# Kernel optimization log

Measured on AMD Instinct MI355X. Metric: run time of the kernel, lower is better.

Reference implementation:

```python
import jax, jax.numpy as jnp
import numpy as np

B, T, I, H, O = 32, 2048, 128, 512, 128
FORGET_BIAS = 1.0


def setup_inputs() -> dict:
    key = jax.random.key(0)
    ks = jax.random.split(key, 8)
    s_ih = 1.0 / np.sqrt(H)
    data = jax.random.normal(ks[0], (B, T, I), dtype=jnp.float32)
    h0 = jnp.zeros((B, H), dtype=jnp.float32)
    c0 = jnp.zeros((B, H), dtype=jnp.float32)
    W_ih = jax.random.uniform(ks[1], (4 * H, I), minval=-s_ih, maxval=s_ih, dtype=jnp.float32)
    W_hh = jax.random.uniform(ks[2], (4 * H, H), minval=-s_ih, maxval=s_ih, dtype=jnp.float32)
    b_ih = jax.random.uniform(ks[3], (4 * H,), minval=-s_ih, maxval=s_ih, dtype=jnp.float32)
    b_hh = jax.random.uniform(ks[4], (4 * H,), minval=-s_ih, maxval=s_ih, dtype=jnp.float32)
    # forget-gate bias init: slice [H:2H] of each bias filled with forget_bias/2
    b_ih = b_ih.at[H:2 * H].set(FORGET_BIAS / 2)
    b_hh = b_hh.at[H:2 * H].set(FORGET_BIAS / 2)
    lin_W = jax.random.uniform(ks[5], (O, H), minval=-s_ih, maxval=s_ih, dtype=jnp.float32)
    lin_b = jax.random.uniform(ks[6], (O,), minval=-s_ih, maxval=s_ih, dtype=jnp.float32)
    return dict(data=data, h0=h0, c0=c0, W_ih=W_ih, W_hh=W_hh,
                b_ih=b_ih, b_hh=b_hh, lin_W=lin_W, lin_b=lin_b)


def reference(data, h0, c0, W_ih, W_hh, b_ih, b_hh, lin_W, lin_b):
    # LSTMCell loop over time (batch_first). PyTorch gate order: i, f, g, o.
    # Original code appends the CELL state (variable `hidden` = c) to hs and
    # decodes from the stacked cell states — reproduced faithfully.
    bias = b_ih + b_hh  # [4H]

    def step(carry, x_t):
        h, c = carry
        gates = x_t @ W_ih.T + h @ W_hh.T + bias  # [B, 4H]
        i_g, f_g, g_g, o_g = jnp.split(gates, 4, axis=-1)
        c_new = jax.nn.sigmoid(f_g) * c + jax.nn.sigmoid(i_g) * jnp.tanh(g_g)
        h_new = jax.nn.sigmoid(o_g) * jnp.tanh(c_new)
        return (h_new, c_new), c_new

    xs = jnp.swapaxes(data, 0, 1)  # [T, B, I]
    (h_f, c_f), cs = jax.lax.scan(step, (h0, c0), xs)
    output = jnp.swapaxes(cs, 0, 1)  # [B, T, H]
    decoded = output @ lin_W.T + lin_b  # [B, T, O]
    return decoded, h_f, c_f
```

## Files before the change

kernel.cpp:

```cpp
#include <hip/hip_runtime.h>
#include <hip/hip_bf16.h>


#define B_ 32
#define T_ 2048
#define I_ 128
#define H_ 512
#define O_ 128
#define NG 8
#define BPG 4
#define WPG 32
#define NWG 256
#define NTHR 512
#define NBUF 4

#define HXS 656
#define CPS 520
#define CAN 0xAAAAAAAAu

typedef short bf16x8 __attribute__((ext_vector_type(8)));
typedef float f32x4 __attribute__((ext_vector_type(4)));
typedef unsigned long long u64;

static __device__ __forceinline__ unsigned f2bf(float f) {
  unsigned u = __float_as_uint(f);
  u = u + 0x7FFFu + ((u >> 16) & 1u);
  return u >> 16;
}
static __device__ __forceinline__ float bf2f(unsigned h) {
  return __uint_as_float(h << 16);
}
static __device__ __forceinline__ float fsigm(float x) {
  return 1.0f / (1.0f + __expf(-x));
}
static __device__ __forceinline__ float ftanh(float x) {
  return 1.0f - 2.0f / (__expf(2.0f * x) + 1.0f);
}

#define ALD(p) __hip_atomic_load((p), __ATOMIC_RELAXED, __HIP_MEMORY_SCOPE_AGENT)
#define AST(p, v) __hip_atomic_store((p), (v), __ATOMIC_RELAXED, __HIP_MEMORY_SCOPE_AGENT)
#define BARRIER() asm volatile("s_waitcnt lgkmcnt(0)\ns_barrier" ::: "memory")

__global__ __launch_bounds__(NTHR, 2) void lstm_fused(
    const float* __restrict__ data, const float* __restrict__ h0,
    const float* __restrict__ c0, const float* __restrict__ W_ih,
    const float* __restrict__ W_hh, const float* __restrict__ b_ih,
    const float* __restrict__ b_hh, const float* __restrict__ lin_W,
    const float* __restrict__ lin_b, float* __restrict__ out,
    float* __restrict__ ws) {
  __shared__ alignas(16) unsigned short sHxHi[BPG * HXS];
  __shared__ alignas(16) unsigned short sHxLo[BPG * HXS];
  __shared__ alignas(16) float sCp[2][BPG * CPS];
  __shared__ alignas(16) float sLinW[4 * CPS];
  __shared__ alignas(16) float sGates[4][2][68];
  __shared__ float sLinB[4];

  const int bid = blockIdx.x;
  const int g = bid & 7;
  const int wgi = bid >> 3;
  const int b0 = g * BPG;
  const int ubase = wgi * 16;
  const int tid = threadIdx.x;
  const int lane = tid & 63;
  const int w = tid >> 6;
  const int gate = w >> 1;
  const int kh = w & 1;
  const int m16 = lane & 15;
  const int kcg = lane >> 4;

  u64* hcPk = (u64*)ws;
  int* cnt = (int*)(ws + (size_t)NBUF * NG * BPG * H_ * 2);

  bf16x8 fAhi[10], fAlo[10];
  const int grow = gate * H_ + ubase + m16;
#pragma unroll
  for (int kk = 0; kk < 10; kk++) {
    int k = kh * 320 + kk * 32 + kcg * 8;
    const float* src = (k < H_) ? (W_hh + (size_t)grow * H_ + k)
                                : (W_ih + (size_t)grow * I_ + (k - H_));
    float4 v0 = *(const float4*)src;
    float4 v1 = *(const float4*)(src + 4);
    float w8[8] = {v0.x, v0.y, v0.z, v0.w, v1.x, v1.y, v1.z, v1.w};
    union { unsigned short u[8]; bf16x8 v; } hi, lo;
#pragma unroll
    for (int j = 0; j < 8; j++) {
      unsigned h = f2bf(w8[j]);
      hi.u[j] = (unsigned short)h;
      lo.u[j] = (unsigned short)f2bf(w8[j] - bf2f(h));
    }
    fAhi[kk] = hi.v;
    fAlo[kk] = lo.v;
  }
  float bias_[4], c_state = 0.f;
  if (tid < 64) {
    int up = tid >> 2, b = tid & 3;
#pragma unroll
    for (int ga = 0; ga < 4; ga++) {
      int r = ga * H_ + ubase + up;
      bias_[ga] = b_ih[r] + b_hh[r];
    }
    c_state = c0[(size_t)(b0 + b) * H_ + ubase + up];
  }
  for (int idx = tid; idx < 4 * H_; idx += NTHR) {
    int o = idx >> 9, k = idx & (H_ - 1);
    sLinW[o * CPS + k] = lin_W[(size_t)(wgi * 4 + o) * H_ + k];
  }
  if (tid < 4) sLinB[tid] = lin_b[wgi * 4 + tid];

  if (tid < 256) {
    int b = tid >> 6, off = (tid & 63) * 8;
    const float* src = h0 + (size_t)(b0 + b) * H_ + off;
    float4 v0 = *(const float4*)src;
    float4 v1 = *(const float4*)(src + 4);
    float w8[8] = {v0.x, v0.y, v0.z, v0.w, v1.x, v1.y, v1.z, v1.w};
    union { unsigned short u[8]; uint4 q; } hi, lo;
#pragma unroll
    for (int j = 0; j < 8; j++) {
      unsigned h = f2bf(w8[j]);
      hi.u[j] = (unsigned short)h;
      lo.u[j] = (unsigned short)f2bf(w8[j] - bf2f(h));
    }
    *(uint4*)&sHxHi[b * HXS + off] = hi.q;
    *(uint4*)&sHxLo[b * HXS + off] = lo.q;
  }
  if (tid >= 256 && tid < 384) {
    int i = tid - 256, b = i >> 5, c4 = i & 31;
    float4 v = *(const float4*)(data + ((size_t)(b0 + b) * T_) * I_ + c4 * 4);
    float w4[4] = {v.x, v.y, v.z, v.w};
    union { unsigned short u[4]; uint2 q; } hi, lo;
#pragma unroll
    for (int j = 0; j < 4; j++) {
      unsigned h = f2bf(w4[j]);
      hi.u[j] = (unsigned short)h;
      lo.u[j] = (unsigned short)f2bf(w4[j] - bf2f(h));
    }
    *(uint2*)&sHxHi[b * HXS + H_ + c4 * 4] = hi.q;
    *(uint2*)&sHxLo[b * HXS + H_ + c4 * 4] = lo.q;
  }
  float4 pfx;
  if (tid >= 320 && tid < 448) {
    int i = tid - 320, b = i >> 5, c4 = i & 31;
    int tp = (T_ > 1) ? 1 : 0;
    pfx = *(const float4*)(data + ((size_t)(b0 + b) * T_ + tp) * I_ + c4 * 4);
  }
  if (tid < 256) {
    int buf = tid >> 6, q = tid & 63, up = q >> 2, b = q & 3;
    AST(&hcPk[(((size_t)buf * NG + g) * BPG + b) * H_ + ubase + up],
        0xAAAAAAAAAAAAAAAAull);
  }
  asm volatile("s_waitcnt vmcnt(0)" ::: "memory");
  __syncthreads();
  if (tid == 0)
    __hip_atomic_fetch_add(&cnt[g * 16], 1, __ATOMIC_RELAXED,
                           __HIP_MEMORY_SCOPE_AGENT);
  if (tid < 64) {
    while (ALD(&cnt[g * 16]) < WPG) {}
  }
  __syncthreads();

  const int bcl = (m16 < BPG) ? m16 : (BPG - 1);
  const unsigned short* pBhi = sHxHi + bcl * HXS + kh * 320 + kcg * 8;
  const unsigned short* pBlo = sHxLo + bcl * HXS + kh * 320 + kcg * 8;

  for (int t = 0; t < T_; t++) {
    f32x4 a0 = {0.f, 0.f, 0.f, 0.f}, a1 = a0, a2 = a0;
#pragma unroll
    for (int kk = 0; kk < 10; kk++) {
      bf16x8 bh = *(const bf16x8*)(pBhi + kk * 32);
      bf16x8 bl = *(const bf16x8*)(pBlo + kk * 32);
      a0 = __builtin_amdgcn_mfma_f32_16x16x32_bf16(fAhi[kk], bh, a0, 0, 0, 0);
      a1 = __builtin_amdgcn_mfma_f32_16x16x32_bf16(fAhi[kk], bl, a1, 0, 0, 0);
      a2 = __builtin_amdgcn_mfma_f32_16x16x32_bf16(fAlo[kk], bh, a2, 0, 0, 0);
    }
    if (m16 < BPG) {
#pragma unroll
      for (int j = 0; j < 4; j++) {
        sGates[gate][kh][kcg * 16 + j * 4 + m16] = a0[j] + a1[j] + a2[j];
      }
    }
    BARRIER();

    if (tid < 64) {
      int up = tid >> 2, b = tid & 3;
      float gi = sGates[0][0][tid] + sGates[0][1][tid] + bias_[0];
      float gf = sGates[1][0][tid] + sGates[1][1][tid] + bias_[1];
      float gg = sGates[2][0][tid] + sGates[2][1][tid] + bias_[2];
      float go = sGates[3][0][tid] + sGates[3][1][tid] + bias_[3];
      float cn = fsigm(gf) * c_state + fsigm(gi) * ftanh(gg);
      float hn = fsigm(go) * ftanh(cn);
      c_state = cn;
      unsigned hh = f2bf(hn);
      unsigned hl = f2bf(hn - bf2f(hh));
      u64 pay = ((u64)__float_as_uint(cn) << 32) | (u64)((hh << 16) | hl);
      AST(&hcPk[(((size_t)(t & 3) * NG + g) * BPG + b) * H_ + ubase + up], pay);
      if (t == T_ - 1) {
        const size_t DEC = (size_t)B_ * T_ * O_;
        out[DEC + (size_t)(b0 + b) * H_ + ubase + up] = hn;
        out[DEC + (size_t)B_ * H_ + (size_t)(b0 + b) * H_ + ubase + up] = cn;
      }
    } else if (tid < 320) {
      if (t > 0) {
        int q = (tid >> 4) - 4;
        int ks = tid & 15;
        int o = q >> 2, b = q & 3;
        const float* cp = sCp[(t & 1) ^ 1];
        float s = 0.f;
#pragma unroll
        for (int j = 0; j < 32; j++) {
          int k = ks + j * 16;
          s += sLinW[o * CPS + k] * cp[b * CPS + k];
        }
        s += __shfl_xor(s, 1);
        s += __shfl_xor(s, 2);
        s += __shfl_xor(s, 4);
        s += __shfl_xor(s, 8);
        if (ks == 0)
          out[((size_t)(b0 + b) * T_ + (t - 1)) * O_ + wgi * 4 + o] =
              s + sLinB[o];
      }
    } else if (tid < 448) {
      int i = tid - 320, b = i >> 5, c4 = i & 31;
      union { unsigned short u[4]; uint2 q; } hi, lo;
      float w4[4] = {pfx.x, pfx.y, pfx.z, pfx.w};
#pragma unroll
      for (int j = 0; j < 4; j++) {
        unsigned h = f2bf(w4[j]);
        hi.u[j] = (unsigned short)h;
        lo.u[j] = (unsigned short)f2bf(w4[j] - bf2f(h));
      }
      *(uint2*)&sHxHi[b * HXS + H_ + c4 * 4] = hi.q;
      *(uint2*)&sHxLo[b * HXS + H_ + c4 * 4] = lo.q;
      int tp = (t + 2 < T_) ? t + 2 : T_ - 1;
      pfx = *(const float4*)(data + ((size_t)(b0 + b) * T_ + tp) * I_ + c4 * 4);
    } else {
      if (t >= 2) {
        int q = tid - 448, up7 = q >> 2, b7 = q & 3;
        AST(&hcPk[(((size_t)((t - 2) & 3) * NG + g) * BPG + b7) * H_ + ubase +
                  up7],
            0xAAAAAAAAAAAAAAAAull);
        asm volatile("s_waitcnt vmcnt(0)" ::: "memory");
      }
    }

    {
      int b = tid >> 7, u4 = (tid & 127) * 4;
      const u64* sp =
          hcPk + (((size_t)(t & 3) * NG + g) * BPG + b) * H_ + u4;
      u64 v0, v1, v2, v3;
      for (;;) {
        v0 = ALD(sp);
        v1 = ALD(sp + 1);
        v2 = ALD(sp + 2);
        v3 = ALD(sp + 3);
        if (((unsigned)v0 != CAN) & ((unsigned)v1 != CAN) &
            ((unsigned)v2 != CAN) & ((unsigned)v3 != CAN))
          break;
      }
      unsigned p0 = (unsigned)v0, p1 = (unsigned)v1, p2 = (unsigned)v2,
               p3 = (unsigned)v3;
      uint2 hw = {(p0 >> 16) | (p1 & 0xFFFF0000u),
                  (p2 >> 16) | (p3 & 0xFFFF0000u)};
      uint2 lw = {(p0 & 0xFFFFu) | (p1 << 16),
                  (p2 & 0xFFFFu) | (p3 << 16)};
      *(uint2*)&sHxHi[b * HXS + u4] = hw;
      *(uint2*)&sHxLo[b * HXS + u4] = lw;
      float4 cf = {__uint_as_float((unsigned)(v0 >> 32)),
                   __uint_as_float((unsigned)(v1 >> 32)),
                   __uint_as_float((unsigned)(v2 >> 32)),
                   __uint_as_float((unsigned)(v3 >> 32))};
      *(float4*)&sCp[t & 1][b * CPS + u4] = cf;
    }
    BARRIER();
  }

  {
    int q = tid >> 5, ks = tid & 31, o = q >> 2, b = q & 3;
    const float* cp = sCp[(T_ - 1) & 1];
    float s = 0.f;
#pragma unroll
    for (int j = 0; j < 16; j++) {
      int k = ks + j * 32;
      s += sLinW[o * CPS + k] * cp[b * CPS + k];
    }
    s += __shfl_xor(s, 1);
    s += __shfl_xor(s, 2);
    s += __shfl_xor(s, 4);
    s += __shfl_xor(s, 8);
    s += __shfl_xor(s, 16);
    if (ks == 0)
      out[((size_t)(b0 + b) * T_ + (T_ - 1)) * O_ + wgi * 4 + o] =
          s + sLinB[o];
  }
}

extern "C" void kernel_launch(void* const* d_in, const int* in_sizes, int n_in,
                              void* d_out, int out_size, void* d_ws, size_t ws_size,
                              hipStream_t stream) {
  const float* data = (const float*)d_in[0];
  const float* h0 = (const float*)d_in[1];
  const float* c0 = (const float*)d_in[2];
  const float* W_ih = (const float*)d_in[3];
  const float* W_hh = (const float*)d_in[4];
  const float* b_ih = (const float*)d_in[5];
  const float* b_hh = (const float*)d_in[6];
  const float* lin_W = (const float*)d_in[7];
  const float* lin_b = (const float*)d_in[8];
  float* out = (float*)d_out;
  float* ws = (float*)d_ws;

  const size_t CNT_OFF = (size_t)NBUF * NG * BPG * H_ * 8;
  hipMemsetAsync((char*)d_ws + CNT_OFF, 0, NG * 16 * sizeof(int), stream);

  hipLaunchKernelGGL(lstm_fused, dim3(NWG), dim3(NTHR), 0, stream, data, h0, c0,
                     W_ih, W_hh, b_ih, b_hh, lin_W, lin_b, out, ws);
}
```

Baseline: 5.505 ms.

## Replace canary-reset handoff with epoch tags embedded in cell-state bits

The cross-workgroup h/c exchange now marks each packed value with a 2-bit epoch tag stored in the low mantissa bits of the cell state, instead of polling for a canary pattern. This removes the per-step canary reset stores and their waitcnt, the startup counter barrier, and the host memset. The first poll loads are also issued right after the MFMA loop so their latency overlaps the gate epilogue. In exchange, the cell values used for decoding lose two mantissa bits. Correctness relies on stale workspace contents not carrying a matching tag.

New measurement: 5.917 ms. 1.07x slower.

```diff
diff --git a/kernel.cpp b/kernel.cpp
--- a/kernel.cpp
+++ b/kernel.cpp
@@ -16,7 +16,6 @@
 
 #define HXS 656
 #define CPS 520
-#define CAN 0xAAAAAAAAu
 
 typedef short bf16x8 __attribute__((ext_vector_type(8)));
 typedef float f32x4 __attribute__((ext_vector_type(4)));
@@ -69,7 +68,6 @@
   const int kcg = lane >> 4;
 
   u64* hcPk = (u64*)ws;
-  int* cnt = (int*)(ws + (size_t)NBUF * NG * BPG * H_ * 2);
 
   bf16x8 fAhi[10], fAlo[10];
   const int grow = gate * H_ + ubase + m16;
@@ -143,19 +141,6 @@
     int tp = (T_ > 1) ? 1 : 0;
     pfx = *(const float4*)(data + ((size_t)(b0 + b) * T_ + tp) * I_ + c4 * 4);
   }
-  if (tid < 256) {
-    int buf = tid >> 6, q = tid & 63, up = q >> 2, b = q & 3;
-    AST(&hcPk[(((size_t)buf * NG + g) * BPG + b) * H_ + ubase + up],
-        0xAAAAAAAAAAAAAAAAull);
-  }
-  asm volatile("s_waitcnt vmcnt(0)" ::: "memory");
-  __syncthreads();
-  if (tid == 0)
-    __hip_atomic_fetch_add(&cnt[g * 16], 1, __ATOMIC_RELAXED,
-                           __HIP_MEMORY_SCOPE_AGENT);
-  if (tid < 64) {
-    while (ALD(&cnt[g * 16]) < WPG) {}
-  }
   __syncthreads();
 
   const int bcl = (m16 < BPG) ? m16 : (BPG - 1);
@@ -163,6 +148,7 @@
   const unsigned short* pBlo = sHxLo + bcl * HXS + kh * 320 + kcg * 8;
 
   for (int t = 0; t < T_; t++) {
+    const unsigned tag = (unsigned)(((t >> 2) + 1) & 3);
     f32x4 a0 = {0.f, 0.f, 0.f, 0.f}, a1 = a0, a2 = a0;
 #pragma unroll
     for (int kk = 0; kk < 10; kk++) {
@@ -172,6 +158,12 @@
       a1 = __builtin_amdgcn_mfma_f32_16x16x32_bf16(fAhi[kk], bl, a1, 0, 0, 0);
       a2 = __builtin_amdgcn_mfma_f32_16x16x32_bf16(fAlo[kk], bh, a2, 0, 0, 0);
     }
+
+    const int sb = tid >> 7;
+    const int su4 = (tid & 127) * 4;
+    const u64* sp = hcPk + (((size_t)(t & 3) * NG + g) * BPG + sb) * H_ + su4;
+    u64 v0 = ALD(sp), v1 = ALD(sp + 1), v2 = ALD(sp + 2), v3 = ALD(sp + 3);
+
     if (m16 < BPG) {
 #pragma unroll
       for (int j = 0; j < 4; j++) {
@@ -191,7 +183,8 @@
       c_state = cn;
       unsigned hh = f2bf(hn);
       unsigned hl = f2bf(hn - bf2f(hh));
-      u64 pay = ((u64)__float_as_uint(cn) << 32) | (u64)((hh << 16) | hl);
+      unsigned cbits = (__float_as_uint(cn) & ~3u) | tag;
+      u64 pay = ((u64)cbits << 32) | (u64)((hh << 16) | hl);
       AST(&hcPk[(((size_t)(t & 3) * NG + g) * BPG + b) * H_ + ubase + up], pay);
       if (t == T_ - 1) {
         const size_t DEC = (size_t)B_ * T_ * O_;
@@ -232,43 +225,33 @@
       *(uint2*)&sHxLo[b * HXS + H_ + c4 * 4] = lo.q;
       int tp = (t + 2 < T_) ? t + 2 : T_ - 1;
       pfx = *(const float4*)(data + ((size_t)(b0 + b) * T_ + tp) * I_ + c4 * 4);
-    } else {
-      if (t >= 2) {
-        int q = tid - 448, up7 = q >> 2, b7 = q & 3;
-        AST(&hcPk[(((size_t)((t - 2) & 3) * NG + g) * BPG + b7) * H_ + ubase +
-                  up7],
-            0xAAAAAAAAAAAAAAAAull);
-        asm volatile("s_waitcnt vmcnt(0)" ::: "memory");
-      }
-    }
-
+    }
+
+    for (;;) {
+      bool bad = (((unsigned)(v0 >> 32) & 3) != tag) |
+                 (((unsigned)(v1 >> 32) & 3) != tag) |
+                 (((unsigned)(v2 >> 32) & 3) != tag) |
+                 (((unsigned)(v3 >> 32) & 3) != tag);
+      if (!bad) break;
+      v0 = ALD(sp);
+      v1 = ALD(sp + 1);
+      v2 = ALD(sp + 2);
+      v3 = ALD(sp + 3);
+    }
     {
-      int b = tid >> 7, u4 = (tid & 127) * 4;
-      const u64* sp =
-          hcPk + (((size_t)(t & 3) * NG + g) * BPG + b) * H_ + u4;
-      u64 v0, v1, v2, v3;
-      for (;;) {
-        v0 = ALD(sp);
-        v1 = ALD(sp + 1);
-        v2 = ALD(sp + 2);
-        v3 = ALD(sp + 3);
-        if (((unsigned)v0 != CAN) & ((unsigned)v1 != CAN) &
-            ((unsigned)v2 != CAN) & ((unsigned)v3 != CAN))
-          break;
-      }
       unsigned p0 = (unsigned)v0, p1 = (unsigned)v1, p2 = (unsigned)v2,
                p3 = (unsigned)v3;
       uint2 hw = {(p0 >> 16) | (p1 & 0xFFFF0000u),
                   (p2 >> 16) | (p3 & 0xFFFF0000u)};
       uint2 lw = {(p0 & 0xFFFFu) | (p1 << 16),
                   (p2 & 0xFFFFu) | (p3 << 16)};
-      *(uint2*)&sHxHi[b * HXS + u4] = hw;
-      *(uint2*)&sHxLo[b * HXS + u4] = lw;
-      float4 cf = {__uint_as_float((unsigned)(v0 >> 32)),
-                   __uint_as_float((unsigned)(v1 >> 32)),
-                   __uint_as_float((unsigned)(v2 >> 32)),
-                   __uint_as_float((unsigned)(v3 >> 32))};
-      *(float4*)&sCp[t & 1][b * CPS + u4] = cf;
+      *(uint2*)&sHxHi[sb * HXS + su4] = hw;
+      *(uint2*)&sHxLo[sb * HXS + su4] = lw;
+      float4 cf = {__uint_as_float((unsigned)(v0 >> 32) & ~3u),
+                   __uint_as_float((unsigned)(v1 >> 32) & ~3u),
+                   __uint_as_float((unsigned)(v2 >> 32) & ~3u),
+                   __uint_as_float((unsigned)(v3 >> 32) & ~3u)};
+      *(float4*)&sCp[t & 1][sb * CPS + su4] = cf;
     }
     BARRIER();
   }
@@ -308,9 +291,6 @@
   float* out = (float*)d_out;
   float* ws = (float*)d_ws;
 
-  const size_t CNT_OFF = (size_t)NBUF * NG * BPG * H_ * 8;
-  hipMemsetAsync((char*)d_ws + CNT_OFF, 0, NG * 16 * sizeof(int), stream);
-
   hipLaunchKernelGGL(lstm_fused, dim3(NWG), dim3(NTHR), 0, stream, data, h0, c0,
                      W_ih, W_hh, b_ih, b_hh, lin_W, lin_b, out, ws);
 }
```
